# Performance work log

Measured on AMD Instinct MI355X. Metric: run time of the kernel, lower is better.

The kernel has to match this reference:

```python
import jax, jax.numpy as jnp
import numpy as np
from jax import lax

N, C, H, W = 5, 256, 128, 128
RATIO = 16
KS = 3
SIGMA = 1.0
THRE = 0.01


def _conv2d_same(x, w):
    k = w.shape[-1]
    p = (k - 1) // 2
    return lax.conv_general_dilated(x, w, (1, 1), [(p, p), (p, p)],
                                    dimension_numbers=('NCHW', 'OIHW', 'NCHW'))


def _gaussian2d():
    c = KS // 2
    x, y = np.mgrid[-c:KS - c, -c:KS - c]
    g = 1.0 / (2.0 * np.pi * SIGMA) * np.exp(-(x ** 2 + y ** 2) / (2.0 * SIGMA ** 2))
    return jnp.asarray(g, jnp.float32).reshape(1, 1, KS, KS)


def _gaussian1d():
    x = np.arange(-(KS - 1) // 2, (KS + 1) // 2, dtype=np.float32)
    g = np.exp(-x ** 2 / (2.0 * SIGMA ** 2))
    g = g / g.sum()
    return jnp.asarray(g, jnp.float32).reshape(1, 1, KS)


def setup_inputs() -> dict:
    key = jax.random.key(0)
    ks = jax.random.split(key, 12)
    s = 0.05
    return {
        'feat': jax.random.normal(ks[0], (N, C, H, W), jnp.float32),
        'mlp_w1': jax.random.normal(ks[1], (C // RATIO, C), jnp.float32) * s,
        'mlp_w2': jax.random.normal(ks[2], (C, C // RATIO), jnp.float32) * s,
        'sp_req_w': jax.random.normal(ks[3], (1, 2, 3, 3), jnp.float32) * s,
        'ch_fus_w': jax.random.normal(ks[4], (C, 2 * C), jnp.float32) * s,
        'sp_fus_w': jax.random.normal(ks[5], (1, 2), jnp.float32) * s,
        'st_w1': jax.random.normal(ks[6], (4 * C, 2 * C), jnp.float32) * s,
        'st_b1': jax.random.normal(ks[7], (4 * C,), jnp.float32) * s,
        'st_w2': jax.random.normal(ks[8], (4 * C, 4 * C), jnp.float32) * s,
        'st_b2': jax.random.normal(ks[9], (4 * C,), jnp.float32) * s,
        'st_w3': jax.random.normal(ks[10], (1, 4 * C), jnp.float32) * s,
        'st_b3': jax.random.normal(ks[11], (1,), jnp.float32) * s,
    }


def _forward(feat, mlp_w1, mlp_w2, sp_req_w, ch_fus_w, sp_fus_w,
             st_w1, st_b1, st_w2, st_b2, st_w3, st_b3):
    g2 = _gaussian2d()
    g1 = _gaussian1d()

    # Channel_Request_Attention: shared MLP on avg- and max-pooled features
    avg = feat.mean(axis=(2, 3))          # [N, C]
    mx = feat.max(axis=(2, 3))            # [N, C]
    mlp = lambda v: jax.nn.relu(v @ mlp_w1.T) @ mlp_w2.T
    ch_att = jax.nn.sigmoid(mlp(avg) + mlp(mx))  # [N, C]

    # Spatial_Request_Attention: 3x3 conv over [mean, max] channel stats
    sp_in = jnp.concatenate([feat.mean(axis=1, keepdims=True),
                             feat.max(axis=1, keepdims=True)], axis=1)  # [N,2,H,W]
    sp_att = jax.nn.sigmoid(_conv2d_same(sp_in, sp_req_w))  # [N,1,H,W]

    # gaussian-smoothed activation map
    act = _conv2d_same(jax.nn.sigmoid(feat.mean(axis=1, keepdims=True)), g2)  # [N,1,H,W]

    ego_ch = 1.0 - ch_att[0]   # [C]
    ego_sp = 1.0 - sp_att[0]   # [1,H,W]

    # channel_fusion: 1x1 conv on concat([ego_request, collaborator_att]) -> split weight
    Wa, Wb = ch_fus_w[:, :C], ch_fus_w[:, C:]
    ch_coef = jax.nn.sigmoid(ego_ch @ Wa.T + ch_att[1:] @ Wb.T)  # [N-1, C]
    # smooth over the channel axis with 1D gaussian
    ch_coef = lax.conv_general_dilated(ch_coef[:, None, :], g1, (1,), [(KS // 2, KS // 2)],
                                       dimension_numbers=('NCH', 'OIH', 'NCH'))[:, 0, :]

    # spatial_fusion: 1x1 conv on concat([ego_sp_request, collaborator_sp_att])
    wa, wb = sp_fus_w[0, 0], sp_fus_w[0, 1]
    sp_coef = jax.nn.sigmoid(wa * ego_sp[None] + wb * sp_att[1:])  # [N-1,1,H,W]
    sp_coef = _conv2d_same(sp_coef, g2)

    sparse_matrix = ch_coef[:, :, None, None] * sp_coef * act[1:]  # [N-1,C,H,W]
    mask = (sparse_matrix > THRE).astype(feat.dtype)
    mean_rate = mask.mean()  # equal-sized per-collaborator means -> global mean

    sparse_feature = jnp.concatenate([feat[:1], feat[1:] * mask], axis=0)  # [N,C,H,W]
    sparse_mask = jnp.concatenate([jnp.ones_like(feat[:1]), mask], axis=0)

    def stat(x):
        h = jax.nn.relu(jnp.einsum('nchw,oc->nohw', x, st_w1) + st_b1[None, :, None, None])
        h = jax.nn.relu(jnp.einsum('nchw,oc->nohw', h, st_w2) + st_b2[None, :, None, None])
        return jnp.einsum('nchw,oc->nohw', h, st_w3) + st_b3[None, :, None, None]

    T = stat(jnp.concatenate([feat, sparse_feature], axis=1))
    feat_prime = jnp.roll(feat, -1, axis=0)
    T_prime = stat(jnp.concatenate([feat_prime, sparse_feature], axis=1))

    joint = (-jax.nn.softplus(-T)).mean()
    marginal = jax.nn.softplus(T_prime).mean()
    total_loss = -(joint - marginal)

    return sparse_feature, total_loss, mean_rate, sparse_mask


def reference(feat, mlp_w1, mlp_w2, sp_req_w, ch_fus_w, sp_fus_w,
              st_w1, st_b1, st_w2, st_b2, st_w3, st_b3):
    return _forward(feat, mlp_w1, mlp_w2, sp_req_w, ch_fus_w, sp_fus_w,
                    st_w1, st_b1, st_w2, st_b2, st_w3, st_b3)
```

## Files before the change

### kernel.cpp

```cpp
#include <hip/hip_runtime.h>
#include <cmath>

#define NIMG 5
#define CCH  256
#define HHH  128
#define WWW  128
#define HW   16384
#define NPIX 81920
#define SF_ELEMS 20971520
#define LOSS_OFF 20971520
#define RATE_OFF 20971521
#define MASK_OFF 20971522

typedef __attribute__((ext_vector_type(4))) float f32x4;
typedef __attribute__((ext_vector_type(8))) __bf16 bf16x8;
typedef __attribute__((ext_vector_type(8))) unsigned short u16x8;

__device__ __forceinline__ unsigned short f32_to_bf16(float f) {
  unsigned int u = __float_as_uint(f);
  u += 0x7FFFu + ((u >> 16) & 1u);
  return (unsigned short)(u >> 16);
}

__device__ __forceinline__ double sigmoid_d(double x) { return 1.0 / (1.0 + exp(-x)); }

__device__ __forceinline__ float softplus_f(float x) {
  if (x > 20.f) return x;
  if (x < -20.f) return expf(x);
  return log1pf(expf(x));
}

__device__ __forceinline__ double g2w(int ky, int kx) {
  int d2 = (ky - 1) * (ky - 1) + (kx - 1) * (kx - 1);
  double g = 0.15915494309189535 * exp(-0.5 * (double)d2);
  return (double)(float)g;
}

__device__ __forceinline__ void gload16(const unsigned short* g, void* l) {
  __builtin_amdgcn_global_load_lds((const __attribute__((address_space(1))) void*)g,
                                   (__attribute__((address_space(3))) void*)l, 16, 0, 0);
}

__global__ void k0_init(double* S1, double* S2, unsigned long long* cnt) {
  if (threadIdx.x == 0 && blockIdx.x == 0) { *S1 = 0.0; *S2 = 0.0; *cnt = 0ull; }
}

__global__ void k1_rednc(const float* __restrict__ feat, double* __restrict__ avg_d,
                         double* __restrict__ mx_d) {
  int nc = blockIdx.x;
  int t = threadIdx.x;
  const float* p = feat + (size_t)nc * HW;
  double s = 0.0;
  float m = -3.4e38f;
  for (int i = t; i < HW; i += 256) { float v = p[i]; s += (double)v; m = fmaxf(m, v); }
  __shared__ double sd[256];
  __shared__ float sm[256];
  sd[t] = s; sm[t] = m;
  __syncthreads();
  for (int o = 128; o > 0; o >>= 1) {
    if (t < o) { sd[t] += sd[t + o]; sm[t] = fmaxf(sm[t], sm[t + o]); }
    __syncthreads();
  }
  if (t == 0) { avg_d[nc] = sd[0] / 16384.0; mx_d[nc] = (double)sm[0]; }
}

__global__ void k2_rednp(const float* __restrict__ feat, double* __restrict__ chmean,
                         double* __restrict__ chmax) {
  int gid = blockIdx.x * 256 + threadIdx.x;
  int n = gid >> 14, p = gid & (HW - 1);
  const float* base = feat + (size_t)n * CCH * HW + p;
  double s = 0.0;
  float m = -3.4e38f;
  for (int c = 0; c < CCH; ++c) { float v = base[(size_t)c * HW]; s += (double)v; m = fmaxf(m, v); }
  chmean[gid] = s / 256.0;
  chmax[gid] = (double)m;
}

__global__ void k3_chan(const double* __restrict__ avg_d, const double* __restrict__ mx_d,
                        const float* __restrict__ w1, const float* __restrict__ w2,
                        const float* __restrict__ fus, double* __restrict__ chcoef_d) {
  __shared__ double hid_a[NIMG][16], hid_m[NIMG][16];
  __shared__ double att[NIMG][CCH];
  __shared__ double sig[4][CCH];
  int t = threadIdx.x;
  if (t < NIMG * 16) {
    int n = t / 16, j = t % 16;
    double sa = 0.0, sx = 0.0;
    for (int c = 0; c < CCH; ++c) {
      double w = (double)w1[j * CCH + c];
      sa += avg_d[n * CCH + c] * w;
      sx += mx_d[n * CCH + c] * w;
    }
    hid_a[n][j] = sa > 0.0 ? sa : 0.0;
    hid_m[n][j] = sx > 0.0 ? sx : 0.0;
  }
  __syncthreads();
  for (int n = 0; n < NIMG; ++n) {
    double oa = 0.0, om = 0.0;
    for (int j = 0; j < 16; ++j) {
      double w = (double)w2[t * 16 + j];
      oa += hid_a[n][j] * w;
      om += hid_m[n][j] * w;
    }
    att[n][t] = sigmoid_d(oa + om);
  }
  __syncthreads();
  for (int m = 0; m < 4; ++m) {
    double s = 0.0;
    for (int k = 0; k < CCH; ++k) {
      s += (1.0 - att[0][k]) * (double)fus[t * 512 + k]
         + att[m + 1][k] * (double)fus[t * 512 + 256 + k];
    }
    sig[m][t] = sigmoid_d(s);
  }
  __syncthreads();
  float a32 = (float)exp(-0.5);
  float s32 = (a32 + 1.0f) + a32;
  double ge = (double)(a32 / s32);
  double gc = (double)(1.0f / s32);
  for (int m = 0; m < 4; ++m) {
    double L = (t > 0) ? sig[m][t - 1] : 0.0;
    double R = (t < 255) ? sig[m][t + 1] : 0.0;
    chcoef_d[m * CCH + t] = ge * L + gc * sig[m][t] + ge * R;
  }
}

__global__ void k4_spatial(const double* __restrict__ chmean, const double* __restrict__ chmax,
                           const float* __restrict__ spw, double* __restrict__ spatt,
                           double* __restrict__ actb) {
  int gid = blockIdx.x * 256 + threadIdx.x;
  int n = gid >> 14, p = gid & (HW - 1);
  int y = p >> 7, x = p & 127;
  const double* cm = chmean + (size_t)n * HW;
  const double* cx = chmax + (size_t)n * HW;
  double s = 0.0, a = 0.0;
  for (int ky = 0; ky < 3; ++ky) {
    int yy = y + ky - 1;
    if ((unsigned)yy >= 128u) continue;
    for (int kx = 0; kx < 3; ++kx) {
      int xx = x + kx - 1;
      if ((unsigned)xx >= 128u) continue;
      int q = (yy << 7) + xx;
      s += (double)spw[ky * 3 + kx] * cm[q] + (double)spw[9 + ky * 3 + kx] * cx[q];
      a += g2w(ky, kx) * sigmoid_d(cm[q]);
    }
  }
  spatt[gid] = sigmoid_d(s);
  actb[gid] = a;
}

__global__ void k5a_spsig(const double* __restrict__ spatt, const float* __restrict__ fus2,
                          double* __restrict__ spsig) {
  int gid = blockIdx.x * 256 + threadIdx.x;
  int m = gid >> 14, p = gid & (HW - 1);
  double wa = (double)fus2[0], wb = (double)fus2[1];
  double ego = 1.0 - spatt[p];
  spsig[gid] = sigmoid_d(wa * ego + wb * spatt[(size_t)(m + 1) * HW + p]);
}

__global__ void k5b_spcoef(const double* __restrict__ spsig, const double* __restrict__ actb,
                           double* __restrict__ spact) {
  int gid = blockIdx.x * 256 + threadIdx.x;
  int m = gid >> 14, p = gid & (HW - 1);
  int y = p >> 7, x = p & 127;
  const double* sp = spsig + (size_t)m * HW;
  double s = 0.0;
  for (int ky = 0; ky < 3; ++ky) {
    int yy = y + ky - 1;
    if ((unsigned)yy >= 128u) continue;
    for (int kx = 0; kx < 3; ++kx) {
      int xx = x + kx - 1;
      if ((unsigned)xx >= 128u) continue;
      s += g2w(ky, kx) * sp[(yy << 7) + xx];
    }
  }
  spact[gid] = s * actb[(size_t)(m + 1) * HW + p];
}

__global__ void k6_mask(const float* __restrict__ feat, const double* __restrict__ chcoef,
                        const double* __restrict__ spact, float* __restrict__ out_sf,
                        float* __restrict__ out_mask, unsigned long long* __restrict__ cnt) {
  const int nth = gridDim.x * blockDim.x;
  int cl = 0;
  for (int g4 = blockIdx.x * blockDim.x + threadIdx.x; g4 < SF_ELEMS / 4; g4 += nth) {
    size_t e = (size_t)g4 * 4;
    int nc = (int)(e >> 14);
    int p = (int)(e & (HW - 1));
    int n = nc >> 8, c = nc & 255;
    f32x4 v = __builtin_nontemporal_load((const f32x4*)&feat[e]);
    f32x4 mk;
    if (n == 0) {
      mk = (f32x4){1.f, 1.f, 1.f, 1.f};
    } else {
      double cc = chcoef[(n - 1) * CCH + c];
      const double* sp = &spact[(size_t)(n - 1) * HW + p];
#pragma unroll
      for (int l = 0; l < 4; ++l) {
        float m = (cc * sp[l] > 0.01) ? 1.f : 0.f;
        mk[l] = m;
        cl += (m != 0.f);
      }
    }
    f32x4 o;
#pragma unroll
    for (int l = 0; l < 4; ++l) o[l] = v[l] * mk[l];
    __builtin_nontemporal_store(o, (f32x4*)&out_sf[e]);
    __builtin_nontemporal_store(mk, (f32x4*)&out_mask[e]);
  }
#pragma unroll
  for (int off = 32; off > 0; off >>= 1) cl += __shfl_down(cl, off);
  if ((threadIdx.x & 63) == 0 && cl > 0) atomicAdd(cnt, (unsigned long long)cl);
}

__global__ void k7_wconv(const float* __restrict__ w1, const float* __restrict__ w2,
                         unsigned short* __restrict__ W1b, unsigned short* __restrict__ W2b) {
  int gid = blockIdx.x * 256 + threadIdx.x;
  if (gid < 524288) W1b[gid] = f32_to_bf16(w1[gid]);
  W2b[gid] = f32_to_bf16(w2[gid]);
}

__global__ void k6b_transpose(const float* __restrict__ feat, const float* __restrict__ sf,
                              unsigned short* __restrict__ featT, unsigned short* __restrict__ sfT) {
  __shared__ unsigned short tf[64][65];
  __shared__ unsigned short tsb[64][65];
  const int bid = blockIdx.x;
  const int n  = bid >> 10;
  const int r  = bid & 1023;
  const int ct = r >> 8;
  const int pt = r & 255;
  const int c0 = ct << 6, p0 = pt << 6;
  const int t = threadIdx.x;
  {
    const int cy = t >> 2, px4 = (t & 3) << 4;
    const float* fp = feat + ((size_t)n * 256 + c0 + cy) * HW + p0 + px4;
    const float* sp = sf   + ((size_t)n * 256 + c0 + cy) * HW + p0 + px4;
#pragma unroll
    for (int i = 0; i < 4; ++i) {
      f32x4 v = *(const f32x4*)(fp + i * 4);
      f32x4 u = *(const f32x4*)(sp + i * 4);
#pragma unroll
      for (int j = 0; j < 4; ++j) {
        tf[cy][px4 + i * 4 + j]  = f32_to_bf16(v[j]);
        tsb[cy][px4 + i * 4 + j] = f32_to_bf16(u[j]);
      }
    }
  }
  __syncthreads();
  {
    const int py = t >> 2, cx = (t & 3) << 4;
    u16x8 o0, o1, q0, q1;
#pragma unroll
    for (int k = 0; k < 8; ++k) { o0[k] = tf[cx + k][py];     q0[k] = tsb[cx + k][py]; }
#pragma unroll
    for (int k = 0; k < 8; ++k) { o1[k] = tf[cx + 8 + k][py]; q1[k] = tsb[cx + 8 + k][py]; }
    size_t ob = ((size_t)n * HW + p0 + py) * 256 + c0 + cx;
    *(u16x8*)&featT[ob]     = o0;
    *(u16x8*)&featT[ob + 8] = o1;
    *(u16x8*)&sfT[ob]       = q0;
    *(u16x8*)&sfT[ob + 8]   = q1;
  }
}

__global__ void kT0_zero(float* __restrict__ T) {
  int g = blockIdx.x * 256 + threadIdx.x;
  for (int i = g; i < 163840; i += gridDim.x * 256) T[i] = 0.f;
}

__global__ __launch_bounds__(256, 2) void k8_gemm1p(
    const unsigned short* __restrict__ featT, const unsigned short* __restrict__ sfT,
    const unsigned short* __restrict__ W1b, const float* __restrict__ b1,
    unsigned short* __restrict__ H1img, int n) {
  __shared__ unsigned short lds[16384];

  const int bid0 = blockIdx.x;
  const int cpx = gridDim.x >> 3;
  const int sb = (bid0 & 7) * cpx + (bid0 >> 3);
  const int mt = sb >> 3, nt = sb & 7;

  const int t = threadIdx.x, l = t & 63, w = t >> 6;
  const int wr = w >> 1, wc = w & 1;
  const int n16 = l & 15, quad = l >> 4;
  const int n1 = (n + 1 == NIMG) ? 0 : n + 1;

  const unsigned short* baseS  = sfT   + ((size_t)n  * HW + mt * 128) * 256;
  const unsigned short* baseF  = featT + ((size_t)n  * HW + mt * 128) * 256;
  const unsigned short* baseF1 = featT + ((size_t)n1 * HW + mt * 128) * 256;
  const unsigned short* baseB  = W1b + (size_t)(nt * 128) * 512;

  const int r0 = l >> 2;
  const int kk = (l & 3) * 8;

  auto stage = [&](int buf, int u) {
    const unsigned short* Ap;
    int kb;
    if (u < 8)       { Ap = baseS  + u * 32;        kb = 256 + u * 32; }
    else if (u < 16) { Ap = baseF  + (u - 8) * 32;  kb = (u - 8) * 32;  }
    else             { Ap = baseF1 + (u - 16) * 32; kb = (u - 16) * 32; }
    const unsigned short* Bp = baseB + kb;
#pragma unroll
    for (int j = 0; j < 2; ++j) {
      const int s = w * 2 + j;
      gload16(Ap + (size_t)(s * 16 + r0) * 256 + kk, (void*)&lds[buf * 4096 + s * 512]);
      gload16(Bp + (size_t)(s * 16 + r0) * 512 + kk, (void*)&lds[8192 + buf * 4096 + s * 512]);
    }
  };

  f32x4 accJ[4][4], accM[4][4];
  {
    f32x4 z = {0.f, 0.f, 0.f, 0.f};
#pragma unroll
    for (int g = 0; g < 4; ++g)
#pragma unroll
      for (int j = 0; j < 4; ++j) accJ[g][j] = z;
  }

  auto kstep = [&](f32x4 (&acc)[4][4], int u, bool last) {
    const int cur = u & 1;
    if (!last) {
      stage(cur ^ 1, u + 1);
      asm volatile("s_waitcnt vmcnt(4)" ::: "memory");
    } else {
      asm volatile("s_waitcnt vmcnt(0)" ::: "memory");
    }
    asm volatile("s_barrier" ::: "memory");
    const int abase = cur * 4096 + (wr * 64) * 32;
    const int bbase = 8192 + cur * 4096 + (wc * 64) * 32;
    bf16x8 af[4], bg[4];
#pragma unroll
    for (int g = 0; g < 4; ++g) af[g] = *(const bf16x8*)&lds[abase + (g * 16 + n16) * 32 + quad * 8];
#pragma unroll
    for (int j = 0; j < 4; ++j) bg[j] = *(const bf16x8*)&lds[bbase + (j * 16 + n16) * 32 + quad * 8];
#pragma unroll
    for (int g = 0; g < 4; ++g)
#pragma unroll
      for (int j = 0; j < 4; ++j)
        acc[g][j] = __builtin_amdgcn_mfma_f32_16x16x32_bf16(af[g], bg[j], acc[g][j], 0, 0, 0);
    asm volatile("s_waitcnt lgkmcnt(0)" ::: "memory");
    asm volatile("s_barrier" ::: "memory");
  };

  stage(0, 0);
  for (int u = 0; u < 8; ++u) kstep(accJ, u, false);
#pragma unroll
  for (int g = 0; g < 4; ++g)
#pragma unroll
    for (int j = 0; j < 4; ++j) accM[g][j] = accJ[g][j];
  for (int u = 8; u < 16; ++u) kstep(accJ, u, false);
  for (int u = 16; u < 24; ++u) kstep(accM, u, u == 23);

  const int colb = nt * 128 + wc * 64;
#pragma unroll
  for (int j = 0; j < 4; ++j) {
    const int col = colb + j * 16 + n16;
    const float bv = b1[col];
#pragma unroll
    for (int g = 0; g < 4; ++g) {
#pragma unroll
      for (int rr = 0; rr < 4; ++rr) {
        const size_t row = (size_t)(mt * 128 + wr * 64 + g * 16 + quad * 4 + rr);
        float vj = accJ[g][j][rr] + bv;
        vj = vj > 0.f ? vj : 0.f;
        H1img[row * 1024 + col] = f32_to_bf16(vj);
        float vm = accM[g][j][rr] + bv;
        vm = vm > 0.f ? vm : 0.f;
        H1img[(row + 16384) * 1024 + col] = f32_to_bf16(vm);
      }
    }
  }
}

__global__ __launch_bounds__(256, 2) void k8_gemm2(
    const unsigned short* __restrict__ H1img, const unsigned short* __restrict__ W2b,
    const float* __restrict__ b2, const float* __restrict__ w3,
    float* __restrict__ Tout, int n) {
  __shared__ unsigned short lds[16384];

  const int bid0 = blockIdx.x;
  const int cpx = gridDim.x >> 3;
  const int sb = (bid0 & 7) * cpx + (bid0 >> 3);
  const int mt = sb >> 3, nt = sb & 7;

  const int t = threadIdx.x, l = t & 63, w = t >> 6;
  const int wr = w >> 1, wc = w & 1;
  const int n16 = l & 15, quad = l >> 4;

  const unsigned short* base_a = H1img + (size_t)(mt * 128) * 1024;
  const unsigned short* base_b = W2b + (size_t)(nt * 128) * 1024;

  const int r0 = l >> 2;
  const int kk = (l & 3) * 8;

  auto stage = [&](int buf, int ts) {
    const unsigned short* Ap = base_a + ts * 32;
    const unsigned short* Bp = base_b + ts * 32;
#pragma unroll
    for (int j = 0; j < 2; ++j) {
      const int s = w * 2 + j;
      gload16(Ap + (size_t)(s * 16 + r0) * 1024 + kk, (void*)&lds[buf * 4096 + s * 512]);
      gload16(Bp + (size_t)(s * 16 + r0) * 1024 + kk, (void*)&lds[8192 + buf * 4096 + s * 512]);
    }
  };

  f32x4 acc[4][4];
  {
    f32x4 z = {0.f, 0.f, 0.f, 0.f};
#pragma unroll
    for (int g = 0; g < 4; ++g)
#pragma unroll
      for (int j = 0; j < 4; ++j) acc[g][j] = z;
  }

  stage(0, 0);
  for (int ts = 0; ts < 32; ++ts) {
    const int cur = ts & 1;
    if (ts + 1 < 32) {
      stage(cur ^ 1, ts + 1);
      asm volatile("s_waitcnt vmcnt(4)" ::: "memory");
    } else {
      asm volatile("s_waitcnt vmcnt(0)" ::: "memory");
    }
    asm volatile("s_barrier" ::: "memory");

    const int abase = cur * 4096 + (wr * 64) * 32;
    const int bbase = 8192 + cur * 4096 + (wc * 64) * 32;
    bf16x8 af[4], bg[4];
#pragma unroll
    for (int g = 0; g < 4; ++g) af[g] = *(const bf16x8*)&lds[abase + (g * 16 + n16) * 32 + quad * 8];
#pragma unroll
    for (int j = 0; j < 4; ++j) bg[j] = *(const bf16x8*)&lds[bbase + (j * 16 + n16) * 32 + quad * 8];
#pragma unroll
    for (int g = 0; g < 4; ++g)
#pragma unroll
      for (int j = 0; j < 4; ++j)
        acc[g][j] = __builtin_amdgcn_mfma_f32_16x16x32_bf16(af[g], bg[j], acc[g][j], 0, 0, 0);

    asm volatile("s_waitcnt lgkmcnt(0)" ::: "memory");
    asm volatile("s_barrier" ::: "memory");
  }

  const int colb = nt * 128 + wc * 64;
  float rs[4][4];
#pragma unroll
  for (int g = 0; g < 4; ++g)
#pragma unroll
    for (int rr = 0; rr < 4; ++rr) rs[g][rr] = 0.f;
#pragma unroll
  for (int j = 0; j < 4; ++j) {
    const int col = colb + j * 16 + n16;
    const float bv = b2[col];
    const float wv = w3[col];
#pragma unroll
    for (int g = 0; g < 4; ++g) {
#pragma unroll
      for (int rr = 0; rr < 4; ++rr) {
        float v = acc[g][j][rr] + bv;
        v = v > 0.f ? v : 0.f;
        rs[g][rr] += v * wv;
      }
    }
  }
#pragma unroll
  for (int off = 1; off < 16; off <<= 1) {
#pragma unroll
    for (int g = 0; g < 4; ++g)
#pragma unroll
      for (int rr = 0; rr < 4; ++rr) rs[g][rr] += __shfl_xor(rs[g][rr], off);
  }
  if (n16 == 0) {
    const int rbase = (mt < 128) ? (n * HW + mt * 128) : (NPIX + n * HW + (mt - 128) * 128);
#pragma unroll
    for (int g = 0; g < 4; ++g)
#pragma unroll
      for (int rr = 0; rr < 4; ++rr)
        atomicAdd(&Tout[rbase + wr * 64 + g * 16 + quad * 4 + rr], rs[g][rr]);
  }
}

__global__ void k8c_red(const float* __restrict__ T, const float* __restrict__ b3,
                        double* __restrict__ S1, double* __restrict__ S2) {
  const int gid = blockIdx.x * 256 + threadIdx.x;
  const int stride = gridDim.x * 256;
  const float bv = b3[0];
  double s1 = 0.0, s2 = 0.0;
  for (int r = gid; r < 163840; r += stride) {
    float Tv = T[r] + bv;
    if (r < NPIX) s1 += (double)softplus_f(-Tv);
    else          s2 += (double)softplus_f(Tv);
  }
#pragma unroll
  for (int off = 32; off > 0; off >>= 1) {
    s1 += __shfl_down(s1, off);
    s2 += __shfl_down(s2, off);
  }
  __shared__ double l1[4], l2[4];
  const int wv = threadIdx.x >> 6;
  if ((threadIdx.x & 63) == 0) { l1[wv] = s1; l2[wv] = s2; }
  __syncthreads();
  if (threadIdx.x == 0) {
    atomicAdd(S1, l1[0] + l1[1] + l1[2] + l1[3]);
    atomicAdd(S2, l2[0] + l2[1] + l2[2] + l2[3]);
  }
}

__device__ __forceinline__ int xidx(int row, int c) {
  return row * 512 + ((((c >> 3) ^ (row & 7)) << 3) | (c & 7));
}
__device__ __forceinline__ int hidx(int row, int oc) {
  return 32768 + row * 256 + ((((oc >> 3) ^ (row & 7)) << 3) | (oc & 7));
}

__global__ __launch_bounds__(1024, 4) void k8_stat(
    const float* __restrict__ feat, const float* __restrict__ sf,
    const unsigned short* __restrict__ W1b, const unsigned short* __restrict__ W2b,
    const float* __restrict__ b1, const float* __restrict__ b2,
    const float* __restrict__ w3, const float* __restrict__ b3,
    double* __restrict__ S1, double* __restrict__ S2) {
  __shared__ unsigned short lds[49280];
  float* t_acc = (float*)&lds[49152];

  const int bid = blockIdx.x;
  const int n = bid >> 9;
  const int p0 = (bid & 511) << 5;
  const int n1 = (n + 1 == NIMG) ? 0 : n + 1;

  const int t = threadIdx.x;
  const int lane = t & 63;
  const int w = t >> 6;
  const int n16 = lane & 15;
  const int quad = lane >> 4;

  {
    const int c = t & 511;
    const int half = t >> 9;
    if (t < 64) t_acc[t] = 0.f;
#pragma unroll
    for (int rb = 0; rb < 2; ++rb) {
      const float* s = (c < 256)
          ? feat + ((size_t)(rb ? n1 : n) * CCH + c) * HW + p0
          : sf + ((size_t)n * CCH + (c - 256)) * HW + p0;
      const f32x4* s4 = (const f32x4*)(s + half * 16);
#pragma unroll
      for (int i = 0; i < 4; ++i) {
        f32x4 v = __builtin_nontemporal_load(s4 + i);
        const int prow = rb * 32 + half * 16 + i * 4;
#pragma unroll
        for (int l = 0; l < 4; ++l) lds[xidx(prow + l, c)] = f32_to_bf16(v[l]);
      }
    }
  }
  __syncthreads();

  f32x4 acc2[4][4];
  {
    f32x4 z = {0.f, 0.f, 0.f, 0.f};
#pragma unroll
    for (int g = 0; g < 4; ++g)
#pragma unroll
      for (int jt = 0; jt < 4; ++jt) acc2[g][jt] = z;
  }

  for (int nc = 0; nc < 4; ++nc) {
    f32x4 acc1[4];
    {
      f32x4 z = {0.f, 0.f, 0.f, 0.f};
#pragma unroll
      for (int g = 0; g < 4; ++g) acc1[g] = z;
    }
    const int o = nc * 256 + w * 16 + n16;
    const unsigned short* Wrow = W1b + (size_t)o * 512;
    bf16x8 bnxt = *(const bf16x8*)&Wrow[quad * 8];
    for (int ks = 0; ks < 16; ++ks) {
      bf16x8 b = bnxt;
      if (ks < 15) bnxt = *(const bf16x8*)&Wrow[(ks + 1) * 32 + quad * 8];
      const int cb = ks * 32 + quad * 8;
#pragma unroll
      for (int g = 0; g < 4; ++g) {
        bf16x8 a = *(const bf16x8*)&lds[xidx(g * 16 + n16, cb)];
        acc1[g] = __builtin_amdgcn_mfma_f32_16x16x32_bf16(a, b, acc1[g], 0, 0, 0);
      }
    }
    __syncthreads();

    {
      const float bv = b1[o];
      const int ol = w * 16 + n16;
#pragma unroll
      for (int g = 0; g < 4; ++g) {
#pragma unroll
        for (int r = 0; r < 4; ++r) {
          const int row = g * 16 + quad * 4 + r;
          float v = acc1[g][r] + bv;
          v = v > 0.f ? v : 0.f;
          lds[hidx(row, ol)] = f32_to_bf16(v);
        }
      }
    }
    __syncthreads();

    for (int ksl = 0; ksl < 8; ++ksl) {
      const int ocb = ksl * 32 + quad * 8;
      bf16x8 a[4];
#pragma unroll
      for (int g = 0; g < 4; ++g) a[g] = *(const bf16x8*)&lds[hidx(g * 16 + n16, ocb)];
#pragma unroll
      for (int jt = 0; jt < 4; ++jt) {
        const int o2 = w * 64 + jt * 16 + n16;
        bf16x8 b = *(const bf16x8*)&W2b[(size_t)o2 * 1024 + nc * 256 + ocb];
#pragma unroll
        for (int g = 0; g < 4; ++g)
          acc2[g][jt] = __builtin_amdgcn_mfma_f32_16x16x32_bf16(a[g], b, acc2[g][jt], 0, 0, 0);
      }
    }
  }

  float tp[4][4];
#pragma unroll
  for (int g = 0; g < 4; ++g)
#pragma unroll
    for (int r = 0; r < 4; ++r) tp[g][r] = 0.f;
#pragma unroll
  for (int jt = 0; jt < 4; ++jt) {
    const int o2 = w * 64 + jt * 16 + n16;
    const float bv = b2[o2];
    const float wv = w3[o2];
#pragma unroll
    for (int g = 0; g < 4; ++g) {
#pragma unroll
      for (int r = 0; r < 4; ++r) {
        float v = acc2[g][jt][r] + bv;
        v = v > 0.f ? v : 0.f;
        tp[g][r] += v * wv;
      }
    }
  }
#pragma unroll
  for (int off = 1; off < 16; off <<= 1) {
#pragma unroll
    for (int g = 0; g < 4; ++g)
#pragma unroll
      for (int r = 0; r < 4; ++r) tp[g][r] += __shfl_xor(tp[g][r], off);
  }
  if (n16 == 0) {
#pragma unroll
    for (int g = 0; g < 4; ++g)
#pragma unroll
      for (int r = 0; r < 4; ++r) atomicAdd(&t_acc[g * 16 + quad * 4 + r], tp[g][r]);
  }
  __syncthreads();

  if (t < 64) {
    const float T = t_acc[t] + b3[0];
    float v = (t < 32) ? softplus_f(-T) : softplus_f(T);
#pragma unroll
    for (int off = 16; off > 0; off >>= 1) v += __shfl_down(v, off);
    if (t == 0) atomicAdd(S1, (double)v);
    if (t == 32) atomicAdd(S2, (double)v);
  }
}

__global__ void k9_final(const double* __restrict__ S1, const double* __restrict__ S2,
                         const unsigned long long* __restrict__ cnt, float* __restrict__ out) {
  if (threadIdx.x == 0 && blockIdx.x == 0) {
    out[LOSS_OFF] = (float)(((*S1) + (*S2)) / 81920.0);
    out[RATE_OFF] = (float)((double)(*cnt) / 16777216.0);
  }
}

#define WS_FEATT 8388608ull
#define WS_SFT   50331648ull
#define WS_H1    92274688ull
#define WS_T     176160768ull
#define WS_NEED  176816128ull

extern "C" void kernel_launch(void* const* d_in, const int* in_sizes, int n_in,
                              void* d_out, int out_size, void* d_ws, size_t ws_size,
                              hipStream_t stream) {
  const float* feat     = (const float*)d_in[0];
  const float* mlp_w1   = (const float*)d_in[1];
  const float* mlp_w2   = (const float*)d_in[2];
  const float* sp_req_w = (const float*)d_in[3];
  const float* ch_fus_w = (const float*)d_in[4];
  const float* sp_fus_w = (const float*)d_in[5];
  const float* st_w1    = (const float*)d_in[6];
  const float* st_b1    = (const float*)d_in[7];
  const float* st_w2    = (const float*)d_in[8];
  const float* st_b2    = (const float*)d_in[9];
  const float* st_w3    = (const float*)d_in[10];
  const float* st_b3    = (const float*)d_in[11];
  float* out = (float*)d_out;

  char* ws = (char*)d_ws;
  double* S1     = (double*)(ws + 0);
  double* S2     = (double*)(ws + 8);
  unsigned long long* cnt = (unsigned long long*)(ws + 16);
  double* avg_d  = (double*)(ws + 64);
  double* mx_d   = (double*)(ws + 10304);
  double* chmean = (double*)(ws + 20544);
  double* chmax  = (double*)(ws + 675904);
  double* spatt  = (double*)(ws + 1331264);
  double* actb   = (double*)(ws + 1986624);
  double* chcoef = (double*)(ws + 2652224);
  double* spsig  = (double*)(ws + 2660416);
  double* spact  = (double*)(ws + 3184704);
  unsigned short* W1b = (unsigned short*)(ws + 3708992);
  unsigned short* W2b = (unsigned short*)(ws + 4757568);

  k0_init<<<1, 64, 0, stream>>>(S1, S2, cnt);
  k1_rednc<<<1280, 256, 0, stream>>>(feat, avg_d, mx_d);
  k2_rednp<<<320, 256, 0, stream>>>(feat, chmean, chmax);
  k3_chan<<<1, 256, 0, stream>>>(avg_d, mx_d, mlp_w1, mlp_w2, ch_fus_w, chcoef);
  k4_spatial<<<320, 256, 0, stream>>>(chmean, chmax, sp_req_w, spatt, actb);
  k5a_spsig<<<256, 256, 0, stream>>>(spatt, sp_fus_w, spsig);
  k5b_spcoef<<<256, 256, 0, stream>>>(spsig, actb, spact);
  k7_wconv<<<4096, 256, 0, stream>>>(st_w1, st_w2, W1b, W2b);
  k6_mask<<<2048, 256, 0, stream>>>(feat, chcoef, spact, out, out + MASK_OFF, cnt);

  if (ws_size >= WS_NEED) {
    unsigned short* featT = (unsigned short*)(ws + WS_FEATT);
    unsigned short* sfT   = (unsigned short*)(ws + WS_SFT);
    unsigned short* H1img = (unsigned short*)(ws + WS_H1);
    float* Tb             = (float*)(ws + WS_T);
    k6b_transpose<<<5120, 256, 0, stream>>>(feat, out, featT, sfT);
    kT0_zero<<<160, 256, 0, stream>>>(Tb);
    for (int n = 0; n < NIMG; ++n) {
      k8_gemm1p<<<1024, 256, 0, stream>>>(featT, sfT, W1b, st_b1, H1img, n);
      k8_gemm2<<<2048, 256, 0, stream>>>(H1img, W2b, st_b2, st_w3, Tb, n);
    }
    k8c_red<<<160, 256, 0, stream>>>(Tb, st_b3, S1, S2);
  } else {
    k8_stat<<<2560, 1024, 0, stream>>>(feat, out, W1b, W2b, st_b1, st_b2, st_w3, st_b3, S1, S2);
  }

  k9_final<<<1, 64, 0, stream>>>(S1, S2, cnt, out);
}
```

Baseline: 1.177 ms.

## Restructure gemm2 into 512-thread triple-buffered K=64 pipeline with swizzled LDS

Rewrites the second stat GEMM kernel to use 8 waves per block (2x4 wave grid, 64x32 per wave) instead of 4, with K tiles of 64 and three LDS buffers so loads run two stages ahead. It adds an XOR swizzle on LDS column placement to avoid bank conflicts, and raises wave priority around the MFMA block. The goal is better overlap of global loads with MFMA work and fewer barriers per K element. In exchange, LDS use grows to 96KB per block, which leaves one block per CU.

Result: slower. 1.532 ms (+30.2%).

```diff
diff --git a/kernel.cpp b/kernel.cpp
--- a/kernel.cpp
+++ b/kernel.cpp
@@ -369,11 +369,11 @@
   }
 }
 
-__global__ __launch_bounds__(256, 2) void k8_gemm2(
+__global__ __launch_bounds__(512, 1) void k8_gemm2(
     const unsigned short* __restrict__ H1img, const unsigned short* __restrict__ W2b,
     const float* __restrict__ b2, const float* __restrict__ w3,
     float* __restrict__ Tout, int n) {
-  __shared__ unsigned short lds[16384];
+  __shared__ unsigned short lds[49152];
 
   const int bid0 = blockIdx.x;
   const int cpx = gridDim.x >> 3;
@@ -381,98 +381,116 @@
   const int mt = sb >> 3, nt = sb & 7;
 
   const int t = threadIdx.x, l = t & 63, w = t >> 6;
-  const int wr = w >> 1, wc = w & 1;
+  const int wm = w >> 2, wn = w & 3;
   const int n16 = l & 15, quad = l >> 4;
 
-  const unsigned short* base_a = H1img + (size_t)(mt * 128) * 1024;
-  const unsigned short* base_b = W2b + (size_t)(nt * 128) * 1024;
-
-  const int r0 = l >> 2;
-  const int kk = (l & 3) * 8;
-
-  auto stage = [&](int buf, int ts) {
-    const unsigned short* Ap = base_a + ts * 32;
-    const unsigned short* Bp = base_b + ts * 32;
+  const unsigned short* baseA = H1img + (size_t)(mt * 128) * 1024;
+  const unsigned short* baseB = W2b  + (size_t)(nt * 128) * 1024;
+
+  const int srow = l >> 3;
+  const int scol = ((l & 7) ^ srow) * 8;
+
+  auto stage = [&](int kt) {
+    const int b = kt % 3;
+    const int k0 = kt * 64;
 #pragma unroll
     for (int j = 0; j < 2; ++j) {
-      const int s = w * 2 + j;
-      gload16(Ap + (size_t)(s * 16 + r0) * 1024 + kk, (void*)&lds[buf * 4096 + s * 512]);
-      gload16(Bp + (size_t)(s * 16 + r0) * 1024 + kk, (void*)&lds[8192 + buf * 4096 + s * 512]);
+      const int rb = j * 64 + w * 8;
+      gload16(baseA + (size_t)(rb + srow) * 1024 + k0 + scol,
+              (void*)&lds[b * 8192 + rb * 64]);
+      gload16(baseB + (size_t)(rb + srow) * 1024 + k0 + scol,
+              (void*)&lds[24576 + b * 8192 + rb * 64]);
     }
   };
 
-  f32x4 acc[4][4];
+  f32x4 acc[4][2];
   {
     f32x4 z = {0.f, 0.f, 0.f, 0.f};
 #pragma unroll
-    for (int g = 0; g < 4; ++g)
-#pragma unroll
-      for (int j = 0; j < 4; ++j) acc[g][j] = z;
-  }
-
-  stage(0, 0);
-  for (int ts = 0; ts < 32; ++ts) {
-    const int cur = ts & 1;
-    if (ts + 1 < 32) {
-      stage(cur ^ 1, ts + 1);
+    for (int M = 0; M < 4; ++M)
+#pragma unroll
+      for (int N = 0; N < 2; ++N) acc[M][N] = z;
+  }
+
+  stage(0);
+  stage(1);
+  const int swz = (n16 & 7) * 8;
+  for (int kt = 0; kt < 16; ++kt) {
+    __builtin_amdgcn_sched_barrier(0);
+    asm volatile("s_waitcnt lgkmcnt(0)" ::: "memory");
+    if (kt + 1 < 16) {
       asm volatile("s_waitcnt vmcnt(4)" ::: "memory");
     } else {
       asm volatile("s_waitcnt vmcnt(0)" ::: "memory");
     }
     asm volatile("s_barrier" ::: "memory");
-
-    const int abase = cur * 4096 + (wr * 64) * 32;
-    const int bbase = 8192 + cur * 4096 + (wc * 64) * 32;
-    bf16x8 af[4], bg[4];
-#pragma unroll
-    for (int g = 0; g < 4; ++g) af[g] = *(const bf16x8*)&lds[abase + (g * 16 + n16) * 32 + quad * 8];
-#pragma unroll
-    for (int j = 0; j < 4; ++j) bg[j] = *(const bf16x8*)&lds[bbase + (j * 16 + n16) * 32 + quad * 8];
-#pragma unroll
-    for (int g = 0; g < 4; ++g)
-#pragma unroll
-      for (int j = 0; j < 4; ++j)
-        acc[g][j] = __builtin_amdgcn_mfma_f32_16x16x32_bf16(af[g], bg[j], acc[g][j], 0, 0, 0);
-
-    asm volatile("s_waitcnt lgkmcnt(0)" ::: "memory");
-    asm volatile("s_barrier" ::: "memory");
-  }
-
-  const int colb = nt * 128 + wc * 64;
+    __builtin_amdgcn_sched_barrier(0);
+    if (kt + 2 < 16) stage(kt + 2);
+
+    const int ab = (kt % 3) * 8192;
+    const int bb = 24576 + (kt % 3) * 8192;
+    bf16x8 aF[4][2], bF[2][2];
+#pragma unroll
+    for (int M = 0; M < 4; ++M) {
+      const int R = wm * 64 + M * 16 + n16;
+#pragma unroll
+      for (int ks = 0; ks < 2; ++ks)
+        aF[M][ks] = *(const bf16x8*)&lds[ab + R * 64 + ((ks * 32 + quad * 8) ^ swz)];
+    }
+#pragma unroll
+    for (int N = 0; N < 2; ++N) {
+      const int C = wn * 32 + N * 16 + n16;
+#pragma unroll
+      for (int ks = 0; ks < 2; ++ks)
+        bF[N][ks] = *(const bf16x8*)&lds[bb + C * 64 + ((ks * 32 + quad * 8) ^ swz)];
+    }
+    __builtin_amdgcn_s_setprio(1);
+#pragma unroll
+    for (int M = 0; M < 4; ++M)
+#pragma unroll
+      for (int N = 0; N < 2; ++N) {
+        acc[M][N] = __builtin_amdgcn_mfma_f32_16x16x32_bf16(aF[M][0], bF[N][0], acc[M][N], 0, 0, 0);
+        acc[M][N] = __builtin_amdgcn_mfma_f32_16x16x32_bf16(aF[M][1], bF[N][1], acc[M][N], 0, 0, 0);
+      }
+    __builtin_amdgcn_s_setprio(0);
+  }
+
   float rs[4][4];
 #pragma unroll
-  for (int g = 0; g < 4; ++g)
-#pragma unroll
-    for (int rr = 0; rr < 4; ++rr) rs[g][rr] = 0.f;
-#pragma unroll
-  for (int j = 0; j < 4; ++j) {
-    const int col = colb + j * 16 + n16;
+  for (int M = 0; M < 4; ++M)
+#pragma unroll
+    for (int rr = 0; rr < 4; ++rr) rs[M][rr] = 0.f;
+#pragma unroll
+  for (int N = 0; N < 2; ++N) {
+    const int col = nt * 128 + wn * 32 + N * 16 + n16;
     const float bv = b2[col];
     const float wv = w3[col];
 #pragma unroll
-    for (int g = 0; g < 4; ++g) {
+    for (int M = 0; M < 4; ++M) {
 #pragma unroll
       for (int rr = 0; rr < 4; ++rr) {
-        float v = acc[g][j][rr] + bv;
+        float v = acc[M][N][rr] + bv;
         v = v > 0.f ? v : 0.f;
-        rs[g][rr] += v * wv;
+        rs[M][rr] += v * wv;
       }
     }
   }
 #pragma unroll
   for (int off = 1; off < 16; off <<= 1) {
 #pragma unroll
-    for (int g = 0; g < 4; ++g)
-#pragma unroll
-      for (int rr = 0; rr < 4; ++rr) rs[g][rr] += __shfl_xor(rs[g][rr], off);
+    for (int M = 0; M < 4; ++M)
+#pragma unroll
+      for (int rr = 0; rr < 4; ++rr) rs[M][rr] += __shfl_xor(rs[M][rr], off);
   }
   if (n16 == 0) {
-    const int rbase = (mt < 128) ? (n * HW + mt * 128) : (NPIX + n * HW + (mt - 128) * 128);
-#pragma unroll
-    for (int g = 0; g < 4; ++g)
+    const int mrow0 = mt * 128;
+    const int rbase = (mrow0 < 16384) ? (n * HW + mrow0)
+                                      : (NPIX + n * HW + (mrow0 - 16384));
+#pragma unroll
+    for (int M = 0; M < 4; ++M)
 #pragma unroll
       for (int rr = 0; rr < 4; ++rr)
-        atomicAdd(&Tout[rbase + wr * 64 + g * 16 + quad * 4 + rr], rs[g][rr]);
+        atomicAdd(&Tout[rbase + wm * 64 + M * 16 + quad * 4 + rr], rs[M][rr]);
   }
 }
 
@@ -724,7 +742,7 @@
     kT0_zero<<<160, 256, 0, stream>>>(Tb);
     for (int n = 0; n < NIMG; ++n) {
       k8_gemm1p<<<1024, 256, 0, stream>>>(featT, sfT, W1b, st_b1, H1img, n);
-      k8_gemm2<<<2048, 256, 0, stream>>>(H1img, W2b, st_b2, st_w3, Tb, n);
+      k8_gemm2<<<2048, 512, 0, stream>>>(H1img, W2b, st_b2, st_w3, Tb, n);
     }
     k8c_red<<<160, 256, 0, stream>>>(Tb, st_b3, S1, S2);
   } else {
```
